# Performance work log

Hardware: AMD Instinct MI355X
Metric: run time of the kernel (lower is better)

Reference implementation:

```python
import jax, jax.numpy as jnp
import numpy as np

NUM_HEADS = 16


def setup_inputs() -> dict:
    key = jax.random.key(0)
    ks = jax.random.split(key, 7)
    B_, N, C = 512, 64, 512
    x = jax.random.normal(ks[0], (B_, N, C), dtype=jnp.float32)
    attn_bias = jax.random.normal(ks[1], (NUM_HEADS, N, N), dtype=jnp.float32)
    mask = jax.random.normal(ks[2], (B_, N, N), dtype=jnp.float32)
    qkv_w = jax.random.normal(ks[3], (3 * C, C), dtype=jnp.float32) * (C ** -0.5)
    qkv_b = jax.random.normal(ks[4], (3 * C,), dtype=jnp.float32) * 0.02
    proj_w = jax.random.normal(ks[5], (C, C), dtype=jnp.float32) * (C ** -0.5)
    proj_b = jax.random.normal(ks[6], (C,), dtype=jnp.float32) * 0.02
    return {"x": x, "attn_bias": attn_bias, "mask": mask,
            "qkv_w": qkv_w, "qkv_b": qkv_b, "proj_w": proj_w, "proj_b": proj_b}


def reference(x, attn_bias, mask, qkv_w, qkv_b, proj_w, proj_b):
    B_, N, C = x.shape
    H = NUM_HEADS
    hd = C // H
    scale = hd ** -0.5
    # qkv projection: (B_, N, 3, H, hd) -> (3, B_, H, N, hd)
    qkv = (x @ qkv_w.T + qkv_b).reshape(B_, N, 3, H, hd)
    qkv = jnp.transpose(qkv, (2, 0, 3, 1, 4))
    q, k, v = qkv[0], qkv[1], qkv[2]
    attn = jnp.einsum('bhnd,bhmd->bhnm', q * scale, k)  # (B_, H, N, N)
    attn = attn + attn_bias            # (H, N, N) broadcasts over batch
    attn = attn + mask[:, None]        # (B_, 1, N, N)
    attn = jax.nn.softmax(attn, axis=-1)
    out = jnp.einsum('bhnm,bhmd->bhnd', attn, v)
    out = jnp.transpose(out, (0, 2, 1, 3)).reshape(B_, N, C)
    return out @ proj_w.T + proj_b
```

## Files before the change

### kernel.cpp

```cpp
#include <hip/hip_runtime.h>
#include <stdint.h>

typedef __attribute__((ext_vector_type(8))) __bf16 bf16x8;
typedef __attribute__((ext_vector_type(4))) float f32x4;
typedef __attribute__((ext_vector_type(4))) float fl4;
typedef __attribute__((ext_vector_type(8))) unsigned short us8;
typedef __attribute__((ext_vector_type(4))) unsigned short us4;

__device__ __forceinline__ unsigned short f2bf(float f) {
  union { float f; unsigned int u; } v;
  v.f = f;
  unsigned int r = v.u + 0x7FFFu + ((v.u >> 16) & 1u);
  return (unsigned short)(r >> 16);
}

#define GLOAD_LDS16(g, l)                                                   \
  __builtin_amdgcn_global_load_lds(                                         \
      (__attribute__((address_space(1))) void*)(g),                         \
      (__attribute__((address_space(3))) void*)(l), 16, 0, 0)

__global__ void f32_to_bf16_kernel(const float* __restrict__ in,
                                   unsigned short* __restrict__ out, int n) {
  int i = (blockIdx.x * blockDim.x + threadIdx.x) * 4;
  if (i + 3 < n) {
    fl4 v = *(const fl4*)(in + i);
    us4 o;
    o[0] = f2bf(v[0]);
    o[1] = f2bf(v[1]);
    o[2] = f2bf(v[2]);
    o[3] = f2bf(v[3]);
    *(us4*)(out + i) = o;
  }
}

template <bool OUT_BF16>
__global__ __launch_bounds__(256, 2) void gemm_nt_kernel(
    const unsigned short* __restrict__ A, const unsigned short* __restrict__ B,
    const float* __restrict__ bias, void* __restrict__ Cout, int M, int N,
    int K) {
  __shared__ __align__(16) unsigned short lA[128 * 64];
  __shared__ __align__(16) unsigned short lB[128 * 64];

  const int tid = threadIdx.x;
  const int lane = tid & 63;
  const int wid = tid >> 6;
  const int wr = (wid >> 1) * 64;
  const int wc = (wid & 1) * 64;
  const int bm = blockIdx.x * 128;
  const int bn = blockIdx.y * 128;

  const f32x4 zero4 = {0.f, 0.f, 0.f, 0.f};
  f32x4 acc[4][4];
#pragma unroll
  for (int m = 0; m < 4; ++m)
#pragma unroll
    for (int n = 0; n < 4; ++n) acc[m][n] = zero4;

  const int srow = tid >> 3;
  const int scol = (tid & 7) << 3;
  unsigned short* Ab = (unsigned short*)(A + (size_t)(bm + srow) * K + scol);
  unsigned short* Bb = (unsigned short*)(B + (size_t)(bn + srow) * K + scol);
  unsigned short* lAb = lA + srow * 64 + scol;
  unsigned short* lBb = lB + srow * 64 + scol;

  const int lr = lane & 15;
  const int lk8 = (lane >> 4) * 8;

  const int nkt = K >> 6;
  for (int kt = 0; kt < nkt; ++kt) {
#pragma unroll
    for (int i = 0; i < 4; ++i) {
      GLOAD_LDS16(Ab + (size_t)(i * 32) * K + kt * 64, lAb + i * 32 * 64);
      GLOAD_LDS16(Bb + (size_t)(i * 32) * K + kt * 64, lBb + i * 32 * 64);
    }
    asm volatile("s_waitcnt vmcnt(0)" ::: "memory");
    __syncthreads();
#pragma unroll
    for (int kk = 0; kk < 2; ++kk) {
      bf16x8 af[4], bfr[4];
#pragma unroll
      for (int m = 0; m < 4; ++m)
        af[m] = *(const bf16x8*)(lA + (wr + m * 16 + lr) * 64 + kk * 32 + lk8);
#pragma unroll
      for (int n = 0; n < 4; ++n)
        bfr[n] = *(const bf16x8*)(lB + (wc + n * 16 + lr) * 64 + kk * 32 + lk8);
#pragma unroll
      for (int m = 0; m < 4; ++m)
#pragma unroll
        for (int n = 0; n < 4; ++n)
          acc[m][n] = __builtin_amdgcn_mfma_f32_16x16x32_bf16(af[m], bfr[n],
                                                              acc[m][n], 0, 0, 0);
    }
    __syncthreads();
  }

  const int crow0 = bm + wr + (lane >> 4) * 4;
  const int ccol0 = bn + wc + lr;
#pragma unroll
  for (int n = 0; n < 4; ++n) {
    const int col = ccol0 + n * 16;
    const float bv = bias[col];
#pragma unroll
    for (int m = 0; m < 4; ++m) {
#pragma unroll
      for (int j = 0; j < 4; ++j) {
        const int row = crow0 + m * 16 + j;
        const float val = acc[m][n][j] + bv;
        if (OUT_BF16)
          ((unsigned short*)Cout)[(size_t)row * N + col] = f2bf(val);
        else
          ((float*)Cout)[(size_t)row * N + col] = val;
      }
    }
  }
}

__global__ __launch_bounds__(256, 2) void attn_kernel(
    const unsigned short* __restrict__ qkv, const float* __restrict__ abias,
    const float* __restrict__ mask, unsigned short* __restrict__ out) {
  __shared__ __align__(16) unsigned short lq[64 * 40];
  __shared__ __align__(16) unsigned short lk[64 * 40];
  __shared__ __align__(16) unsigned short lvT[32 * 72];
  __shared__ __align__(16) float ls[64 * 68];
  __shared__ __align__(16) unsigned short lp[64 * 72];

  const int blk = blockIdx.x;
  const int b = blk >> 4;
  const int h = blk & 15;
  const int tid = threadIdx.x;
  const int lane = tid & 63;
  const int wid = tid >> 6;
  const int lr = lane & 15;
  const int lk8 = (lane >> 4) * 8;

  {
    const int r = tid >> 2;
    const int d0 = (tid & 3) * 8;
    const size_t base = (size_t)(b * 64 + r) * 1536 + h * 32 + d0;
    us8 qv = *(const us8*)(qkv + base);
    us8 kv = *(const us8*)(qkv + base + 512);
    us8 vv = *(const us8*)(qkv + base + 1024);
    *(us8*)(lq + r * 40 + d0) = qv;
    *(us8*)(lk + r * 40 + d0) = kv;
#pragma unroll
    for (int i = 0; i < 8; ++i) lvT[(d0 + i) * 72 + r] = vv[i];
  }
  __syncthreads();

  f32x4 s[4];
  {
    bf16x8 aq = *(const bf16x8*)(lq + (wid * 16 + lr) * 40 + lk8);
#pragma unroll
    for (int n = 0; n < 4; ++n) {
      bf16x8 bk = *(const bf16x8*)(lk + (n * 16 + lr) * 40 + lk8);
      f32x4 z = {0.f, 0.f, 0.f, 0.f};
      s[n] = __builtin_amdgcn_mfma_f32_16x16x32_bf16(aq, bk, z, 0, 0, 0);
    }
  }
  const float scale = 0.17677669529663687f;
  const int sr0 = wid * 16 + (lane >> 4) * 4;
#pragma unroll
  for (int n = 0; n < 4; ++n) {
    const int col = n * 16 + lr;
#pragma unroll
    for (int j = 0; j < 4; ++j) {
      const int row = sr0 + j;
      ls[row * 68 + col] = s[n][j] * scale + abias[(h * 64 + row) * 64 + col] +
                           mask[((size_t)b * 64 + row) * 64 + col];
    }
  }
  __syncthreads();

  {
    const int r = tid >> 2;
    const int c0 = (tid & 3) * 16;
    float e[16];
#pragma unroll
    for (int i = 0; i < 16; ++i) e[i] = ls[r * 68 + c0 + i];
    float mx = e[0];
#pragma unroll
    for (int i = 1; i < 16; ++i) mx = fmaxf(mx, e[i]);
    mx = fmaxf(mx, __shfl_xor(mx, 1));
    mx = fmaxf(mx, __shfl_xor(mx, 2));
    float sum = 0.f;
#pragma unroll
    for (int i = 0; i < 16; ++i) {
      e[i] = __expf(e[i] - mx);
      sum += e[i];
    }
    sum += __shfl_xor(sum, 1);
    sum += __shfl_xor(sum, 2);
    const float inv = 1.f / sum;
#pragma unroll
    for (int i = 0; i < 16; ++i) lp[r * 72 + c0 + i] = f2bf(e[i] * inv);
  }
  __syncthreads();

  f32x4 o[2];
  o[0] = (f32x4){0.f, 0.f, 0.f, 0.f};
  o[1] = o[0];
#pragma unroll
  for (int kk = 0; kk < 2; ++kk) {
    bf16x8 pa = *(const bf16x8*)(lp + (wid * 16 + lr) * 72 + kk * 32 + lk8);
#pragma unroll
    for (int d = 0; d < 2; ++d) {
      bf16x8 vb = *(const bf16x8*)(lvT + (d * 16 + lr) * 72 + kk * 32 + lk8);
      o[d] = __builtin_amdgcn_mfma_f32_16x16x32_bf16(pa, vb, o[d], 0, 0, 0);
    }
  }
#pragma unroll
  for (int d = 0; d < 2; ++d) {
    const int col = h * 32 + d * 16 + lr;
#pragma unroll
    for (int j = 0; j < 4; ++j) {
      const int row = sr0 + j;
      out[(size_t)(b * 64 + row) * 512 + col] = f2bf(o[d][j]);
    }
  }
}

extern "C" void kernel_launch(void* const* d_in, const int* in_sizes, int n_in,
                              void* d_out, int out_size, void* d_ws,
                              size_t ws_size, hipStream_t stream) {
  (void)in_sizes; (void)n_in; (void)out_size; (void)ws_size;
  const float* x = (const float*)d_in[0];
  const float* abias = (const float*)d_in[1];
  const float* mask = (const float*)d_in[2];
  const float* qkv_w = (const float*)d_in[3];
  const float* qkv_b = (const float*)d_in[4];
  const float* proj_w = (const float*)d_in[5];
  const float* proj_b = (const float*)d_in[6];

  char* ws = (char*)d_ws;
  unsigned short* ws_x = (unsigned short*)(ws);
  unsigned short* ws_qkv = (unsigned short*)(ws + 33554432);
  unsigned short* ws_wq = (unsigned short*)(ws + 134217728);
  unsigned short* ws_wp = (unsigned short*)(ws + 135790592);
  unsigned short* ws_att = ws_x;

  f32_to_bf16_kernel<<<16384, 256, 0, stream>>>(x, ws_x, 16777216);
  f32_to_bf16_kernel<<<768, 256, 0, stream>>>(qkv_w, ws_wq, 786432);
  f32_to_bf16_kernel<<<256, 256, 0, stream>>>(proj_w, ws_wp, 262144);

  gemm_nt_kernel<true><<<dim3(256, 12), 256, 0, stream>>>(
      ws_x, ws_wq, qkv_b, ws_qkv, 32768, 1536, 512);

  attn_kernel<<<8192, 256, 0, stream>>>(ws_qkv, abias, mask, ws_att);

  gemm_nt_kernel<false><<<dim3(256, 4), 256, 0, stream>>>(
      ws_att, ws_wp, proj_b, d_out, 32768, 512, 512);
}
```

Baseline: 294.2 us.

## Replace GEMM with 256x256-tile double-buffered swizzled pipelined kernel

Replaces the 128x128 single-buffered GEMM with a 512-thread 256x256 tile kernel. It double-buffers LDS with staged global-to-LDS loads interleaved between MFMA quadrants, XOR-swizzles LDS columns to reduce bank conflicts, and uses s_setprio around MFMA bursts. It also remaps block IDs in groups of 8 for cache locality. The aim is to hide global load latency and raise data reuse, at the cost of 128KB LDS per block, lower occupancy, and a larger tail for the small projection GEMM (256 blocks).

After: 310.1 us. 1.05x slower.

```diff
diff --git a/kernel.cpp b/kernel.cpp
--- a/kernel.cpp
+++ b/kernel.cpp
@@ -16,8 +16,10 @@
 
 #define GLOAD_LDS16(g, l)                                                   \
   __builtin_amdgcn_global_load_lds(                                         \
-      (__attribute__((address_space(1))) void*)(g),                         \
+      (const __attribute__((address_space(1))) void*)(g),                   \
       (__attribute__((address_space(3))) void*)(l), 16, 0, 0)
+
+#define MEMFENCE asm volatile("" ::: "memory")
 
 __global__ void f32_to_bf16_kernel(const float* __restrict__ in,
                                    unsigned short* __restrict__ out, int n) {
@@ -34,74 +36,179 @@
 }
 
 template <bool OUT_BF16>
-__global__ __launch_bounds__(256, 2) void gemm_nt_kernel(
+__global__ __launch_bounds__(512, 2) void gemm256_kernel(
     const unsigned short* __restrict__ A, const unsigned short* __restrict__ B,
     const float* __restrict__ bias, void* __restrict__ Cout, int M, int N,
     int K) {
-  __shared__ __align__(16) unsigned short lA[128 * 64];
-  __shared__ __align__(16) unsigned short lB[128 * 64];
+  __shared__ __align__(16) unsigned short lds[65536];
+  char* ldsA = (char*)lds;
+  char* ldsB = (char*)lds + 65536;
 
   const int tid = threadIdx.x;
   const int lane = tid & 63;
   const int wid = tid >> 6;
-  const int wr = (wid >> 1) * 64;
-  const int wc = (wid & 1) * 64;
-  const int bm = blockIdx.x * 128;
-  const int bn = blockIdx.y * 128;
-
-  const f32x4 zero4 = {0.f, 0.f, 0.f, 0.f};
-  f32x4 acc[4][4];
-#pragma unroll
-  for (int m = 0; m < 4; ++m)
-#pragma unroll
-    for (int n = 0; n < 4; ++n) acc[m][n] = zero4;
+  const int wm = wid >> 2;
+  const int wn = wid & 3;
+  const int lr = lane & 15;
+  const int lg = lane >> 4;
+
+  const int nwg = gridDim.x;
+  const int cpx = nwg >> 3;
+  const int bid = blockIdx.x;
+  const int id2 = (bid & 7) * cpx + (bid >> 3);
+  const int MT = M >> 8;
+  const int bm = (id2 % MT) << 8;
+  const int bn = (id2 / MT) << 8;
+
+  const int nkt = K >> 6;
 
   const int srow = tid >> 3;
-  const int scol = (tid & 7) << 3;
-  unsigned short* Ab = (unsigned short*)(A + (size_t)(bm + srow) * K + scol);
-  unsigned short* Bb = (unsigned short*)(B + (size_t)(bn + srow) * K + scol);
-  unsigned short* lAb = lA + srow * 64 + scol;
-  unsigned short* lBb = lB + srow * 64 + scol;
-
-  const int lr = lane & 15;
-  const int lk8 = (lane >> 4) * 8;
-
-  const int nkt = K >> 6;
+  const int scolb = (((tid & 7) << 4) ^ ((srow & 7) << 4));
+  const char* Ab = (const char*)A;
+  const char* Bb = (const char*)B;
+
+#define STAGE_A(kt2, q)                                                        \
+  GLOAD_LDS16(Ab + ((size_t)(bm + (q)*64 + srow) * K + (kt2)*64) * 2 + scolb,  \
+              ldsA + (((kt2)&1) * 32768) + (q)*8192 + tid * 16)
+#define STAGE_B(kt2, q)                                                        \
+  GLOAD_LDS16(Bb + ((size_t)(bn + (q)*64 + srow) * K + (kt2)*64) * 2 + scolb,  \
+              ldsB + (((kt2)&1) * 32768) + (q)*8192 + tid * 16)
+
+  const int swzb = (lr & 7) << 4;
+  const int lkb = lg << 4;
+  const int ck0 = (0 + lkb) ^ swzb;
+  const int ck1 = (64 + lkb) ^ swzb;
+
+  f32x4 acc[8][4];
+#pragma unroll
+  for (int m = 0; m < 8; ++m)
+#pragma unroll
+    for (int n = 0; n < 4; ++n) acc[m][n] = (f32x4){0.f, 0.f, 0.f, 0.f};
+
+#pragma unroll
+  for (int q = 0; q < 4; ++q) STAGE_A(0, q);
+#pragma unroll
+  for (int q = 0; q < 4; ++q) STAGE_B(0, q);
+#pragma unroll
+  for (int q = 0; q < 4; ++q) STAGE_A(1, q);
+  asm volatile("s_waitcnt vmcnt(4)" ::: "memory");
+  __builtin_amdgcn_s_barrier();
+  MEMFENCE;
+
   for (int kt = 0; kt < nkt; ++kt) {
-#pragma unroll
-    for (int i = 0; i < 4; ++i) {
-      GLOAD_LDS16(Ab + (size_t)(i * 32) * K + kt * 64, lAb + i * 32 * 64);
-      GLOAD_LDS16(Bb + (size_t)(i * 32) * K + kt * 64, lBb + i * 32 * 64);
-    }
-    asm volatile("s_waitcnt vmcnt(0)" ::: "memory");
-    __syncthreads();
-#pragma unroll
-    for (int kk = 0; kk < 2; ++kk) {
-      bf16x8 af[4], bfr[4];
-#pragma unroll
-      for (int m = 0; m < 4; ++m)
-        af[m] = *(const bf16x8*)(lA + (wr + m * 16 + lr) * 64 + kk * 32 + lk8);
-#pragma unroll
-      for (int n = 0; n < 4; ++n)
-        bfr[n] = *(const bf16x8*)(lB + (wc + n * 16 + lr) * 64 + kk * 32 + lk8);
-#pragma unroll
-      for (int m = 0; m < 4; ++m)
-#pragma unroll
-        for (int n = 0; n < 4; ++n)
-          acc[m][n] = __builtin_amdgcn_mfma_f32_16x16x32_bf16(af[m], bfr[n],
-                                                              acc[m][n], 0, 0, 0);
-    }
-    __syncthreads();
-  }
-
-  const int crow0 = bm + wr + (lane >> 4) * 4;
-  const int ccol0 = bn + wc + lr;
+    const int p = kt & 1;
+    const char* rA = ldsA + p * 32768;
+    const char* rB = ldsB + p * 32768;
+    const int arow = (wm * 128 + lr) * 128;
+    const int brow = (wn * 64 + lr) * 128;
+
+    bf16x8 a0[4][2], a1[4][2], b0[2][2], b1[2][2];
+
+#pragma unroll
+    for (int m = 0; m < 4; ++m) {
+      a0[m][0] = *(const bf16x8*)(rA + arow + m * 2048 + ck0);
+      a0[m][1] = *(const bf16x8*)(rA + arow + m * 2048 + ck1);
+    }
+#pragma unroll
+    for (int n = 0; n < 2; ++n) {
+      b0[n][0] = *(const bf16x8*)(rB + brow + n * 2048 + ck0);
+      b0[n][1] = *(const bf16x8*)(rB + brow + n * 2048 + ck1);
+    }
+    if (kt + 1 < nkt) { STAGE_B(kt + 1, 0); STAGE_B(kt + 1, 1); }
+    MEMFENCE;
+    __builtin_amdgcn_s_barrier();
+    MEMFENCE;
+    __builtin_amdgcn_s_setprio(1);
+#pragma unroll
+    for (int m = 0; m < 4; ++m)
+#pragma unroll
+      for (int n = 0; n < 2; ++n) {
+        acc[m][n] = __builtin_amdgcn_mfma_f32_16x16x32_bf16(a0[m][0], b0[n][0], acc[m][n], 0, 0, 0);
+        acc[m][n] = __builtin_amdgcn_mfma_f32_16x16x32_bf16(a0[m][1], b0[n][1], acc[m][n], 0, 0, 0);
+      }
+    __builtin_amdgcn_s_setprio(0);
+    MEMFENCE;
+    __builtin_amdgcn_s_barrier();
+    MEMFENCE;
+
+#pragma unroll
+    for (int n = 0; n < 2; ++n) {
+      b1[n][0] = *(const bf16x8*)(rB + brow + (n + 2) * 2048 + ck0);
+      b1[n][1] = *(const bf16x8*)(rB + brow + (n + 2) * 2048 + ck1);
+    }
+    if (kt + 1 < nkt) { STAGE_B(kt + 1, 2); STAGE_B(kt + 1, 3); }
+    if (kt + 2 < nkt) { STAGE_A(kt + 2, 0); }
+    MEMFENCE;
+    __builtin_amdgcn_s_barrier();
+    MEMFENCE;
+    __builtin_amdgcn_s_setprio(1);
+#pragma unroll
+    for (int m = 0; m < 4; ++m)
+#pragma unroll
+      for (int n = 0; n < 2; ++n) {
+        acc[m][n + 2] = __builtin_amdgcn_mfma_f32_16x16x32_bf16(a0[m][0], b1[n][0], acc[m][n + 2], 0, 0, 0);
+        acc[m][n + 2] = __builtin_amdgcn_mfma_f32_16x16x32_bf16(a0[m][1], b1[n][1], acc[m][n + 2], 0, 0, 0);
+      }
+    __builtin_amdgcn_s_setprio(0);
+    MEMFENCE;
+    __builtin_amdgcn_s_barrier();
+    MEMFENCE;
+
+#pragma unroll
+    for (int m = 0; m < 4; ++m) {
+      a1[m][0] = *(const bf16x8*)(rA + arow + (m + 4) * 2048 + ck0);
+      a1[m][1] = *(const bf16x8*)(rA + arow + (m + 4) * 2048 + ck1);
+    }
+    if (kt + 2 < nkt) { STAGE_A(kt + 2, 2); }
+    MEMFENCE;
+    __builtin_amdgcn_s_barrier();
+    MEMFENCE;
+    __builtin_amdgcn_s_setprio(1);
+#pragma unroll
+    for (int m = 0; m < 4; ++m)
+#pragma unroll
+      for (int n = 0; n < 2; ++n) {
+        acc[m + 4][n] = __builtin_amdgcn_mfma_f32_16x16x32_bf16(a1[m][0], b0[n][0], acc[m + 4][n], 0, 0, 0);
+        acc[m + 4][n] = __builtin_amdgcn_mfma_f32_16x16x32_bf16(a1[m][1], b0[n][1], acc[m + 4][n], 0, 0, 0);
+      }
+    __builtin_amdgcn_s_setprio(0);
+    MEMFENCE;
+    __builtin_amdgcn_s_barrier();
+    MEMFENCE;
+
+    if (kt + 2 < nkt) { STAGE_A(kt + 2, 1); STAGE_A(kt + 2, 3); }
+    MEMFENCE;
+    __builtin_amdgcn_s_barrier();
+    MEMFENCE;
+    __builtin_amdgcn_s_setprio(1);
+#pragma unroll
+    for (int m = 0; m < 4; ++m)
+#pragma unroll
+      for (int n = 0; n < 2; ++n) {
+        acc[m + 4][n + 2] = __builtin_amdgcn_mfma_f32_16x16x32_bf16(a1[m][0], b1[n][0], acc[m + 4][n + 2], 0, 0, 0);
+        acc[m + 4][n + 2] = __builtin_amdgcn_mfma_f32_16x16x32_bf16(a1[m][1], b1[n][1], acc[m + 4][n + 2], 0, 0, 0);
+      }
+    __builtin_amdgcn_s_setprio(0);
+    if (kt + 2 < nkt) {
+      asm volatile("s_waitcnt vmcnt(4)" ::: "memory");
+    } else {
+      asm volatile("s_waitcnt vmcnt(0)" ::: "memory");
+    }
+    __builtin_amdgcn_s_barrier();
+    MEMFENCE;
+  }
+
+#undef STAGE_A
+#undef STAGE_B
+
+  const int crow0 = bm + wm * 128 + lg * 4;
+  const int ccol0 = bn + wn * 64 + lr;
 #pragma unroll
   for (int n = 0; n < 4; ++n) {
     const int col = ccol0 + n * 16;
     const float bv = bias[col];
 #pragma unroll
-    for (int m = 0; m < 4; ++m) {
+    for (int m = 0; m < 8; ++m) {
 #pragma unroll
       for (int j = 0; j < 4; ++j) {
         const int row = crow0 + m * 16 + j;
@@ -242,11 +349,11 @@
   f32_to_bf16_kernel<<<768, 256, 0, stream>>>(qkv_w, ws_wq, 786432);
   f32_to_bf16_kernel<<<256, 256, 0, stream>>>(proj_w, ws_wp, 262144);
 
-  gemm_nt_kernel<true><<<dim3(256, 12), 256, 0, stream>>>(
-      ws_x, ws_wq, qkv_b, ws_qkv, 32768, 1536, 512);
+  gemm256_kernel<true><<<768, 512, 0, stream>>>(ws_x, ws_wq, qkv_b, ws_qkv,
+                                                32768, 1536, 512);
 
   attn_kernel<<<8192, 256, 0, stream>>>(ws_qkv, abias, mask, ws_att);
 
-  gemm_nt_kernel<false><<<dim3(256, 4), 256, 0, stream>>>(
-      ws_att, ws_wp, proj_b, d_out, 32768, 512, 512);
-}
+  gemm256_kernel<false><<<256, 512, 0, stream>>>(ws_att, ws_wp, proj_b, d_out,
+                                                 32768, 512, 512);
+}
```
